# Kernel tuning notes

Hardware: AMD Instinct MI355X
Metric: run time of the kernel (lower is better)

Reference implementation:

```python
import jax, jax.numpy as jnp
import numpy as np
from functools import reduce

NUM_LEAVES = 41   # third-level classes 0..40
N_SECOND = 9      # second-level classes 41..49
N_FIRST = 3       # first-level classes 50..52
NUM_CLASSES = NUM_LEAVES + N_SECOND + N_FIRST  # 53
DEPTH = 3
INTERNAL_START = 41
GAMMA = 2.0
LOSS_WEIGHT = 1.0


def _build_tree():
    # leaf -> second-level parent, second -> first-level parent
    parent2 = INTERNAL_START + np.arange(NUM_LEAVES) % N_SECOND            # in [41,49]
    parent1_of_second = INTERNAL_START + N_SECOND + np.arange(N_SECOND) % N_FIRST  # in [50,52]

    # anc_indexes: (DEPTH, NUM_CLASSES); row 0 = self, rows 1,2 = ancestors (padded with self)
    anc = np.tile(np.arange(NUM_CLASSES), (DEPTH, 1))
    for l in range(NUM_LEAVES):
        anc[1, l] = parent2[l]
        anc[2, l] = parent1_of_second[parent2[l] - INTERNAL_START]
    for c in range(INTERNAL_START, INTERNAL_START + N_SECOND):
        anc[1, c] = parent1_of_second[c - INTERNAL_START]
        anc[2, c] = anc[1, c]
    # first-level classes keep self in all rows

    # multi-hot ancestor table for leaf labels: (NUM_LEAVES, NUM_CLASSES)
    mh = np.zeros((NUM_LEAVES, NUM_CLASSES), dtype=np.int32)
    for l in range(NUM_LEAVES):
        mh[l, [l, parent2[l], parent1_of_second[parent2[l] - INTERNAL_START]]] = 1

    # ragged descendant lists for internal classes 41..52 (include self), padded by repeating first entry
    desc_lists = []
    for c in range(INTERNAL_START, NUM_CLASSES):
        if c < INTERNAL_START + N_SECOND:
            ds = [c] + [l for l in range(NUM_LEAVES) if parent2[l] == c]
        else:
            seconds = [s for s in range(INTERNAL_START, INTERNAL_START + N_SECOND)
                       if parent1_of_second[s - INTERNAL_START] == c]
            leaves = [l for l in range(NUM_LEAVES)
                      if parent1_of_second[parent2[l] - INTERNAL_START] == c]
            ds = [c] + seconds + leaves
        desc_lists.append(ds)
    max_d = max(len(d) for d in desc_lists)
    desc = np.stack([np.array(d + [d[0]] * (max_d - len(d)), dtype=np.int32) for d in desc_lists])
    return anc.astype(np.int32), mh, desc


def setup_inputs() -> dict:
    key = jax.random.key(0)
    k1, k2 = jax.random.split(key)
    B, H, W = 4, 512, 512
    cls_score = jax.random.normal(k1, (B, NUM_CLASSES, H, W), dtype=jnp.float32)
    label = jax.random.randint(k2, (B, H, W), 0, NUM_LEAVES, dtype=jnp.int64)
    anc, mh, desc = _build_tree()
    return {
        "cls_score": cls_score,
        "label": label,
        "anc_indexes": jnp.asarray(anc),      # (3, 53) int32
        "mh_table": jnp.asarray(mh),          # (41, 53) int32 multi-hot ancestor rows
        "desc_table": jnp.asarray(desc),      # (12, max_desc) int32 padded descendants
    }


def reference(cls_score, label, anc_indexes, mh_table, desc_table):
    C = cls_score.shape[1]
    # (B,C,H,W) -> (N,C), matching transpose(1,3).transpose(1,2).reshape(-1,C)
    pred = jnp.transpose(cls_score, (0, 2, 3, 1)).reshape(-1, C)
    lab = label.reshape(-1)
    multi_hot = mh_table[lab]                 # (N, C) int
    mh_bool = multi_hot.astype(bool)

    # min over ancestor chain (row 0 is self): small fixed loop over DEPTH
    mins = pred[:, anc_indexes[0]]
    for d in range(1, anc_indexes.shape[0]):
        mins = jnp.minimum(mins, pred[:, anc_indexes[d]])
    new_pred = jnp.where(mh_bool, mins, pred)

    # max over descendants (from original pred) for internal classes, applied where NOT multi_hot
    maxes = pred[:, desc_table[:, 0]]         # (N, C-41)
    for j in range(1, desc_table.shape[1]):
        maxes = jnp.maximum(maxes, pred[:, desc_table[:, j]])
    internal = new_pred[:, INTERNAL_START:]
    internal = jnp.where(mh_bool[:, INTERNAL_START:], internal, maxes)
    new_pred = jnp.concatenate([new_pred[:, :INTERNAL_START], internal], axis=1)

    # focal BCE-with-logits
    t = multi_hot.astype(new_pred.dtype)
    p = jax.nn.sigmoid(new_pred)
    one_minus_pt = (1.0 - p) * t + p * (1.0 - t)
    focal_w = one_minus_pt ** GAMMA
    # numerically stable BCE with logits
    bce = jnp.maximum(new_pred, 0.0) - new_pred * t + jnp.log1p(jnp.exp(-jnp.abs(new_pred)))
    loss = jnp.mean(bce * focal_w)
    return LOSS_WEIGHT * loss
```

## Files before the change

### kernel.cpp

```cpp
#include <hip/hip_runtime.h>

#define NC      53
#define HW_BITS 18
#define BLK     256
#define PPT     4


__device__ __forceinline__ float focal_term(float y) {
    const float a   = __builtin_amdgcn_exp2f(-1.4426950408889634f * fabsf(y));
    const float l2  = __builtin_amdgcn_logf(1.0f + a);
    const float spp = fmaf(l2, 0.6931471805599453f, fmaxf(y, 0.0f));
    const float spn = fmaf(l2, 0.6931471805599453f, fmaxf(-y, 0.0f));
    const float w   = __builtin_amdgcn_exp2f(-2.8853900817779268f * spn);
    return w * spp;
}

__global__ __launch_bounds__(256) void focal_tree_kernel(
    const float* __restrict__ cls,
    const int4*  __restrict__ label4,
    float* __restrict__ out, float scale)
{
    const int tid = blockIdx.x * BLK + threadIdx.x;
    const int n0  = tid << 2;
    const int b   = n0 >> HW_BITS;
    const int hw  = n0 & ((1 << HW_BITS) - 1);
    const float4* p = (const float4*)(cls + (((size_t)b * NC) << HW_BITS)) + (hw >> 2);

    const int4 lab = label4[tid];
    const int labv[4] = {lab.x, lab.y, lab.z, lab.w};
    int a1v[4], a3v[4];
    #pragma unroll
    for (int k = 0; k < 4; ++k) {
        a1v[k] = 41 + labv[k] % 9;
        a3v[k] = labv[k] % 3;
    }

    float pfir[3][4];
    #pragma unroll
    for (int f = 0; f < 3; ++f) {
        const float4 v = p[(size_t)(50 + f) << 16];
        pfir[f][0]=v.x; pfir[f][1]=v.y; pfir[f][2]=v.z; pfir[f][3]=v.w;
    }

    float acc[4] = {0.f, 0.f, 0.f, 0.f};

    #pragma unroll
    for (int f = 0; f < 3; ++f) {
        float fmax_[4] = {pfir[f][0], pfir[f][1], pfir[f][2], pfir[f][3]};

        #pragma unroll 1
        for (int r = f; r < 9; r += 3) {
            const float4 vs = p[(size_t)(41 + r) << 16];
            const float ps[4] = {vs.x, vs.y, vs.z, vs.w};
            float manc[4], smax[4];
            #pragma unroll
            for (int k = 0; k < 4; ++k) {
                manc[k] = fminf(ps[k], pfir[f][k]);
                smax[k] = ps[k];
            }

            #pragma unroll
            for (int j = 0; j < 5; ++j) {
                const int l = r + 9 * j;
                if (l < 41) {
                    const float4 vl = p[(size_t)l << 16];
                    const float xv[4] = {vl.x, vl.y, vl.z, vl.w};
                    #pragma unroll
                    for (int k = 0; k < 4; ++k) {
                        const float x = xv[k];
                        const float y = (l == labv[k]) ? -fminf(x, manc[k]) : x;
                        acc[k] += focal_term(y);
                        smax[k] = fmaxf(smax[k], x);
                    }
                }
            }

            #pragma unroll
            for (int k = 0; k < 4; ++k) {
                const float y = (a1v[k] == 41 + r) ? -manc[k] : smax[k];
                acc[k] += focal_term(y);
                fmax_[k] = fmaxf(fmax_[k], smax[k]);
            }
        }

        #pragma unroll
        for (int k = 0; k < 4; ++k) {
            const float y = (a3v[k] == f) ? -pfir[f][k] : fmax_[k];
            acc[k] += focal_term(y);
        }
    }

    float v = (acc[0] + acc[1]) + (acc[2] + acc[3]);
    #pragma unroll
    for (int off = 32; off > 0; off >>= 1)
        v += __shfl_down(v, off, 64);

    __shared__ float wsum[4];
    const int lane = threadIdx.x & 63;
    const int wid  = threadIdx.x >> 6;
    if (lane == 0) wsum[wid] = v;
    __syncthreads();
    if (threadIdx.x == 0) {
        const float s = (wsum[0] + wsum[1]) + (wsum[2] + wsum[3]);
        atomicAdd(out, s * scale);
    }
}

extern "C" void kernel_launch(void* const* d_in, const int* in_sizes, int n_in,
                              void* d_out, int out_size, void* d_ws, size_t ws_size,
                              hipStream_t stream) {
    const float* cls    = (const float*)d_in[0];
    const int4*  label4 = (const int4*)d_in[1];
    float* out = (float*)d_out;

    const int npix  = in_sizes[1];
    const float scale = (float)(1.0 / ((double)npix * (double)NC));

    hipMemsetAsync(d_out, 0, sizeof(float), stream);

    const int blocks = npix / (BLK * PPT);
    focal_tree_kernel<<<blocks, BLK, 0, stream>>>(cls, label4, out, scale);
}
```

Before: 311.6 us.

## Software-pipeline class-group loads with double buffering and explicit group scheduling

Replaces the rolled per-second-level-class loop with fully unrolled, templated group stages. Each group's float4 loads are issued one group ahead into two alternating register buffers, so memory latency overlaps focal-term math. It also adds a minimum-occupancy hint of 4 to launch_bounds. The cost is higher register pressure from holding 12 float4 buffers, and the occupancy hint could force spills.

```diff
diff --git a/kernel.cpp b/kernel.cpp
--- a/kernel.cpp
+++ b/kernel.cpp
@@ -15,7 +15,66 @@
     return w * spp;
 }
 
-__global__ __launch_bounds__(256) void focal_tree_kernel(
+
+template<int R>
+__device__ __forceinline__ void load_group(const float4* __restrict__ p,
+                                           float4 (&buf)[6]) {
+    buf[0] = p[(size_t)(41 + R) << 16];
+    buf[1] = p[(size_t)(R +  0) << 16];
+    buf[2] = p[(size_t)(R +  9) << 16];
+    buf[3] = p[(size_t)(R + 18) << 16];
+    buf[4] = p[(size_t)(R + 27) << 16];
+    if constexpr (R + 36 < 41) buf[5] = p[(size_t)(R + 36) << 16];
+}
+
+template<int R>
+__device__ __forceinline__ void compute_group(const float4 (&buf)[6],
+    const int (&labv)[4], const int (&a1v)[4],
+    const float (&pf)[4],
+    float (&fm)[4], float (&acc)[4])
+{
+    const float ps[4] = {buf[0].x, buf[0].y, buf[0].z, buf[0].w};
+    float manc[4], smax[4];
+    #pragma unroll
+    for (int k = 0; k < 4; ++k) {
+        manc[k] = fminf(ps[k], pf[k]);
+        smax[k] = ps[k];
+    }
+
+    constexpr int NL = (R + 36 < 41) ? 5 : 4;
+    #pragma unroll
+    for (int j = 0; j < NL; ++j) {
+        const int l = R + 9 * j;
+        const float xv[4] = {buf[1+j].x, buf[1+j].y, buf[1+j].z, buf[1+j].w};
+        #pragma unroll
+        for (int k = 0; k < 4; ++k) {
+            const float x = xv[k];
+            const float y = (l == labv[k]) ? -fminf(x, manc[k]) : x;
+            acc[k] += focal_term(y);
+            smax[k] = fmaxf(smax[k], x);
+        }
+    }
+
+    #pragma unroll
+    for (int k = 0; k < 4; ++k) {
+        const float y = (a1v[k] == 41 + R) ? -manc[k] : smax[k];
+        acc[k] += focal_term(y);
+        fm[k] = fmaxf(fm[k], smax[k]);
+    }
+}
+
+template<int F>
+__device__ __forceinline__ void emit_first(const float (&pf)[4],
+    const int (&a3v)[4], const float (&fm)[4], float (&acc)[4])
+{
+    #pragma unroll
+    for (int k = 0; k < 4; ++k) {
+        const float y = (a3v[k] == F) ? -pf[k] : fm[k];
+        acc[k] += focal_term(y);
+    }
+}
+
+__global__ __launch_bounds__(256, 4) void focal_tree_kernel(
     const float* __restrict__ cls,
     const int4*  __restrict__ label4,
     float* __restrict__ out, float scale)
@@ -43,52 +102,39 @@
     }
 
     float acc[4] = {0.f, 0.f, 0.f, 0.f};
+    float fm[4];
+    float4 bufA[6], bufB[6];
+
+    load_group<0>(p, bufA);
+    load_group<3>(p, bufB);
 
     #pragma unroll
-    for (int f = 0; f < 3; ++f) {
-        float fmax_[4] = {pfir[f][0], pfir[f][1], pfir[f][2], pfir[f][3]};
+    for (int k = 0; k < 4; ++k) fm[k] = pfir[0][k];
+    compute_group<0>(bufA, labv, a1v, pfir[0], fm, acc);
+    load_group<6>(p, bufA);
+    compute_group<3>(bufB, labv, a1v, pfir[0], fm, acc);
+    load_group<1>(p, bufB);
+    compute_group<6>(bufA, labv, a1v, pfir[0], fm, acc);
+    emit_first<0>(pfir[0], a3v, fm, acc);
 
-        #pragma unroll 1
-        for (int r = f; r < 9; r += 3) {
-            const float4 vs = p[(size_t)(41 + r) << 16];
-            const float ps[4] = {vs.x, vs.y, vs.z, vs.w};
-            float manc[4], smax[4];
-            #pragma unroll
-            for (int k = 0; k < 4; ++k) {
-                manc[k] = fminf(ps[k], pfir[f][k]);
-                smax[k] = ps[k];
-            }
+    #pragma unroll
+    for (int k = 0; k < 4; ++k) fm[k] = pfir[1][k];
+    load_group<4>(p, bufA);
+    compute_group<1>(bufB, labv, a1v, pfir[1], fm, acc);
+    load_group<7>(p, bufB);
+    compute_group<4>(bufA, labv, a1v, pfir[1], fm, acc);
+    load_group<2>(p, bufA);
+    compute_group<7>(bufB, labv, a1v, pfir[1], fm, acc);
+    emit_first<1>(pfir[1], a3v, fm, acc);
 
-            #pragma unroll
-            for (int j = 0; j < 5; ++j) {
-                const int l = r + 9 * j;
-                if (l < 41) {
-                    const float4 vl = p[(size_t)l << 16];
-                    const float xv[4] = {vl.x, vl.y, vl.z, vl.w};
-                    #pragma unroll
-                    for (int k = 0; k < 4; ++k) {
-                        const float x = xv[k];
-                        const float y = (l == labv[k]) ? -fminf(x, manc[k]) : x;
-                        acc[k] += focal_term(y);
-                        smax[k] = fmaxf(smax[k], x);
-                    }
-                }
-            }
-
-            #pragma unroll
-            for (int k = 0; k < 4; ++k) {
-                const float y = (a1v[k] == 41 + r) ? -manc[k] : smax[k];
-                acc[k] += focal_term(y);
-                fmax_[k] = fmaxf(fmax_[k], smax[k]);
-            }
-        }
-
-        #pragma unroll
-        for (int k = 0; k < 4; ++k) {
-            const float y = (a3v[k] == f) ? -pfir[f][k] : fmax_[k];
-            acc[k] += focal_term(y);
-        }
-    }
+    #pragma unroll
+    for (int k = 0; k < 4; ++k) fm[k] = pfir[2][k];
+    load_group<5>(p, bufB);
+    compute_group<2>(bufA, labv, a1v, pfir[2], fm, acc);
+    load_group<8>(p, bufA);
+    compute_group<5>(bufB, labv, a1v, pfir[2], fm, acc);
+    compute_group<8>(bufA, labv, a1v, pfir[2], fm, acc);
+    emit_first<2>(pfir[2], a3v, fm, acc);
 
     float v = (acc[0] + acc[1]) + (acc[2] + acc[3]);
     #pragma unroll
```

Measured after the change: 342.1 us. +9.8%, slower.
